# Optimization experiments

Hardware: AMD Instinct MI355X
Metric: run time of the kernel (lower is better)

Reference implementation:

```python
import jax, jax.numpy as jnp
import numpy as np

B, T, IN = 32, 1024, 256
H = 128          # hidden_size
NL = 2           # num_layers
NC = 4           # num_classes
F2 = 2 * H       # bidirectional feature size


def _lstm_dir(xs, w_ih, w_hh, b_ih, b_hh, reverse):
    # xs: [T, B, in]; w_ih: [4H, in]; w_hh: [4H, H]
    if reverse:
        xs = xs[::-1]
    h0 = jnp.zeros((xs.shape[1], H), xs.dtype)
    c0 = jnp.zeros((xs.shape[1], H), xs.dtype)

    def step(carry, xt):
        h, c = carry
        g = xt @ w_ih.T + b_ih + h @ w_hh.T + b_hh  # [B, 4H]
        i, f, gg, o = jnp.split(g, 4, axis=-1)       # PyTorch gate order i,f,g,o
        c = jax.nn.sigmoid(f) * c + jax.nn.sigmoid(i) * jnp.tanh(gg)
        h = jax.nn.sigmoid(o) * jnp.tanh(c)
        return (h, c), h

    _, hs = jax.lax.scan(step, (h0, c0), xs)  # [T, B, H]
    if reverse:
        hs = hs[::-1]
    return hs


def setup_inputs() -> dict:
    key = jax.random.key(0)
    ks = jax.random.split(key, 12)
    s = 0.05
    x = jax.random.normal(ks[0], (B, T, IN), jnp.float32)
    # stacked LSTM params: [layer, direction, ...]; layer0 in = IN, layer1 in = 2H = IN
    w_ih = jax.random.normal(ks[1], (NL, 2, 4 * H, IN), jnp.float32) * s
    w_hh = jax.random.normal(ks[2], (NL, 2, 4 * H, H), jnp.float32) * s
    b_ih = jax.random.normal(ks[3], (NL, 2, 4 * H), jnp.float32) * s
    b_hh = jax.random.normal(ks[4], (NL, 2, 4 * H), jnp.float32) * s
    wq = jax.random.normal(ks[5], (F2, F2), jnp.float32) * s
    wk = jax.random.normal(ks[6], (F2, F2), jnp.float32) * s
    wv = jax.random.normal(ks[7], (F2, F2), jnp.float32) * s
    bq = jax.random.normal(ks[8], (F2,), jnp.float32) * s
    bk = jax.random.normal(ks[9], (F2,), jnp.float32) * s
    bv = jax.random.normal(ks[10], (F2,), jnp.float32) * s
    w_fc = jax.random.normal(ks[11], (NC, F2), jnp.float32) * s
    b_fc = jnp.zeros((NC,), jnp.float32)
    return {"x": x, "w_ih": w_ih, "w_hh": w_hh, "b_ih": b_ih, "b_hh": b_hh,
            "wq": wq, "wk": wk, "wv": wv, "bq": bq, "bk": bk, "bv": bv,
            "w_fc": w_fc, "b_fc": b_fc}


def reference(x, w_ih, w_hh, b_ih, b_hh, wq, wk, wv, bq, bk, bv, w_fc, b_fc):
    # --- biLSTM (eval mode: inter-layer dropout inactive) ---
    xs = jnp.swapaxes(x, 0, 1)  # time-major [T, B, IN]
    for l in range(NL):
        fwd = _lstm_dir(xs, w_ih[l, 0], w_hh[l, 0], b_ih[l, 0], b_hh[l, 0], False)
        bwd = _lstm_dir(xs, w_ih[l, 1], w_hh[l, 1], b_ih[l, 1], b_hh[l, 1], True)
        xs = jnp.concatenate([fwd, bwd], axis=-1)  # [T, B, 2H]
    out = jnp.swapaxes(xs, 0, 1)  # [B, T, 2H]
    # --- naive full self-attention ---
    q = out @ wq.T + bq
    k = out @ wk.T + bk
    v = out @ wv.T + bv
    scores = jnp.einsum('btd,bsd->bts', q, k) / jnp.sqrt(jnp.float32(F2))
    attn = jax.nn.softmax(scores, axis=-1)          # [B, T, T]
    ctx = jnp.einsum('bts,bsd->btd', attn, v)       # [B, T, 2H]
    # --- FC head on last timestep ---
    return ctx[:, -1, :] @ w_fc.T + b_fc            # [B, NC]
```

## Files before the change

### kernel.cpp

```cpp
#include <hip/hip_runtime.h>
#include <math.h>
#include <stdint.h>

#define BB 32
#define TT 1024
#define HH 128
#define G4 512
#define CH 16
#define XPS 516

typedef _Float16 half2_t __attribute__((ext_vector_type(2)));
typedef _Float16 half8_t __attribute__((ext_vector_type(8)));
typedef float f32x4 __attribute__((ext_vector_type(4)));

__device__ __forceinline__ float fdot2f(half2_t a, half2_t b, float c) {
    return __builtin_amdgcn_fdot2(a, b, c, false);
}
__device__ __forceinline__ float rcpf(float x) {
    return __builtin_amdgcn_rcpf(x);
}
__device__ __forceinline__ float dpp_xor1(float x) {
    return __builtin_bit_cast(float, __builtin_amdgcn_update_dpp(
        0, __builtin_bit_cast(int, x), 0xB1, 0xF, 0xF, true));
}
__device__ __forceinline__ float dpp_xor2(float x) {
    return __builtin_bit_cast(float, __builtin_amdgcn_update_dpp(
        0, __builtin_bit_cast(int, x), 0x4E, 0xF, 0xF, true));
}
__device__ __forceinline__ void bar_lgkm() {
    asm volatile("s_waitcnt lgkmcnt(0)\n\ts_barrier" ::: "memory");
}

__global__ __launch_bounds__(256) void cvt_wih(
    const float* __restrict__ w, _Float16* __restrict__ o)
{
    const int i = (blockIdx.x * 256 + threadIdx.x) * 4;
    float4 f = *(const float4*)(w + i);
    half2_t t[2] = { half2_t{(_Float16)f.x, (_Float16)f.y},
                     half2_t{(_Float16)f.z, (_Float16)f.w} };
    *(float2*)(o + i) = *(float2*)t;
}

__global__ __launch_bounds__(512, 1) void lstm_fused(
    const float* __restrict__ x_in,
    const _Float16* __restrict__ wih16_l,
    const float* __restrict__ b_ih_l,
    const float* __restrict__ b_hh_l,
    const float* __restrict__ w_hh_l,
    float* __restrict__ out)
{
    const int b = blockIdx.x & 31;
    const int d = blockIdx.x >> 5;
    const int tid = threadIdx.x;
    const int wvid = tid >> 6;
    const int l = tid & 63;
    const int s = l & 3;
    const int g = l >> 2;
    const int j = (wvid << 4) | g;

    __shared__ __align__(16) _Float16 hs[HH];
    __shared__ __align__(16) float xp[2][CH * XPS];
    __shared__ __align__(16) half2_t xr[2][CH * 128];
    __shared__ __align__(16) float obuf[CH * HH];

    half2_t wv[4][16];
#pragma unroll
    for (int G = 0; G < 4; ++G) {
        const float* wr = w_hh_l + (size_t)(d * G4 + 128 * G + j) * HH + 32 * s;
#pragma unroll
        for (int q4 = 0; q4 < 8; ++q4) {
            float4 f = *(const float4*)(wr + 4 * q4);
            wv[G][2 * q4]     = half2_t{(_Float16)f.x, (_Float16)f.y};
            wv[G][2 * q4 + 1] = half2_t{(_Float16)f.z, (_Float16)f.w};
        }
    }

    const int acol0 = wvid * 64 + (l & 15);
    const _Float16* wn = wih16_l + ((size_t)d * G4 + acol0) * 256 + (l >> 4) * 8;
    const float bias0 = b_ih_l[d * G4 + acol0]      + b_hh_l[d * G4 + acol0];
    const float bias1 = b_ih_l[d * G4 + acol0 + 16] + b_hh_l[d * G4 + acol0 + 16];
    const float bias2 = b_ih_l[d * G4 + acol0 + 32] + b_hh_l[d * G4 + acol0 + 32];
    const float bias3 = b_ih_l[d * G4 + acol0 + 48] + b_hh_l[d * G4 + acol0 + 48];

    const int cbase = ((acol0 & 127) << 2) + (acol0 >> 7);

    const float* xbase = x_in + (size_t)b * TT * 256;

    const int a_noswz = (l & 15) * 512 + (l >> 4) * 16;
    const int a_swz   = (l & 7) << 4;
    const int w_swz_byte = (tid * 16) ^ (((tid >> 5) & 7) << 4);

#pragma unroll 1
    for (int p = 0; p < 2; ++p) {
        const int tlo = d ? (1008 - p * CH) : p * CH;
        const float* gs = xbase + (size_t)tlo * 256 + tid * 8;
        float4 f0 = *(const float4*)gs;
        float4 f1 = *(const float4*)(gs + 4);
        half2_t t4[4] = { half2_t{(_Float16)f0.x, (_Float16)f0.y},
                          half2_t{(_Float16)f0.z, (_Float16)f0.w},
                          half2_t{(_Float16)f1.x, (_Float16)f1.y},
                          half2_t{(_Float16)f1.z, (_Float16)f1.w} };
        *(float4*)((char*)xr[p] + w_swz_byte) = *(float4*)t4;
    }
    __syncthreads();

    f32x4 acc0 = {bias0, bias0, bias0, bias0};
    f32x4 acc1 = {bias1, bias1, bias1, bias1};
    f32x4 acc2 = {bias2, bias2, bias2, bias2};
    f32x4 acc3 = {bias3, bias3, bias3, bias3};

#pragma unroll
    for (int kt = 0; kt < 8; ++kt) {
        half8_t af = *(const half8_t*)((const char*)xr[0] + ((a_noswz + kt * 64) ^ a_swz));
        acc0 = __builtin_amdgcn_mfma_f32_16x16x32_f16(af, *(const half8_t*)(wn +         kt * 32), acc0, 0, 0, 0);
        acc1 = __builtin_amdgcn_mfma_f32_16x16x32_f16(af, *(const half8_t*)(wn +  4096 + kt * 32), acc1, 0, 0, 0);
        acc2 = __builtin_amdgcn_mfma_f32_16x16x32_f16(af, *(const half8_t*)(wn +  8192 + kt * 32), acc2, 0, 0, 0);
        acc3 = __builtin_amdgcn_mfma_f32_16x16x32_f16(af, *(const half8_t*)(wn + 12288 + kt * 32), acc3, 0, 0, 0);
    }
    {
        const int rb = (l >> 4) * 4;
#pragma unroll
        for (int q = 0; q < 4; ++q) {
            const int ix = (rb + q) * XPS + cbase;
            xp[0][ix]       = acc0[q];
            xp[0][ix + 64]  = acc1[q];
            xp[0][ix + 128] = acc2[q];
            xp[0][ix + 192] = acc3[q];
        }
    }
    acc0 = (f32x4){bias0, bias0, bias0, bias0};
    acc1 = (f32x4){bias1, bias1, bias1, bias1};
    acc2 = (f32x4){bias2, bias2, bias2, bias2};
    acc3 = (f32x4){bias3, bias3, bias3, bias3};

    if (tid < 64) ((half2_t*)hs)[tid] = half2_t{(_Float16)0.f, (_Float16)0.f};
    float c = 0.f;
    float* ob = out + (size_t)b * TT * 256 + d * HH;
    __syncthreads();

    float4 rg0 = {}, rg1 = {};
    half8_t afrag = {};
    for (int ck = 0; ck < 64; ++ck) {
        const int cur = ck & 1;
        const bool doproj = (ck + 1 < 64);
        if (ck + 2 < 64) {
            const int tlo2 = d ? (1008 - (ck + 2) * CH) : (ck + 2) * CH;
            const float* gs = xbase + (size_t)tlo2 * 256 + tid * 8;
            rg0 = *(const float4*)gs;
            rg1 = *(const float4*)(gs + 4);
        }
        const float* xb = xp[cur];
        const char* xr_rd = (const char*)xr[cur ^ 1];

#pragma unroll 1
        for (int si = 0; si < CH; ++si) {
            half8_t bA = {}, bB = {};
            if (doproj) {
                const int kt = si >> 1;
                if (!(si & 1)) {
                    afrag = *(const half8_t*)(xr_rd + ((a_noswz + kt * 64) ^ a_swz));
                    bA = *(const half8_t*)(wn +        kt * 32);
                    bB = *(const half8_t*)(wn + 4096 + kt * 32);
                } else {
                    bA = *(const half8_t*)(wn +  8192 + kt * 32);
                    bB = *(const half8_t*)(wn + 12288 + kt * 32);
                }
            }

            const int lds_t = d ? (CH - 1 - si) : si;

            const float4 xg4 = *(const float4*)&xb[lds_t * XPS + (j << 2)];

            const float4* hp = (const float4*)(hs + 32 * s);
            float4 hA = hp[0], hB = hp[1], hC = hp[2], hD = hp[3];
            half2_t hh[16];
            hh[0]  = __builtin_bit_cast(half2_t, hA.x);
            hh[1]  = __builtin_bit_cast(half2_t, hA.y);
            hh[2]  = __builtin_bit_cast(half2_t, hA.z);
            hh[3]  = __builtin_bit_cast(half2_t, hA.w);
            hh[4]  = __builtin_bit_cast(half2_t, hB.x);
            hh[5]  = __builtin_bit_cast(half2_t, hB.y);
            hh[6]  = __builtin_bit_cast(half2_t, hB.z);
            hh[7]  = __builtin_bit_cast(half2_t, hB.w);
            hh[8]  = __builtin_bit_cast(half2_t, hC.x);
            hh[9]  = __builtin_bit_cast(half2_t, hC.y);
            hh[10] = __builtin_bit_cast(half2_t, hC.z);
            hh[11] = __builtin_bit_cast(half2_t, hC.w);
            hh[12] = __builtin_bit_cast(half2_t, hD.x);
            hh[13] = __builtin_bit_cast(half2_t, hD.y);
            hh[14] = __builtin_bit_cast(half2_t, hD.z);
            hh[15] = __builtin_bit_cast(half2_t, hD.w);

            float a0 = 0.f, a1 = 0.f, a2 = 0.f, a3 = 0.f;
            float e0 = 0.f, e1 = 0.f, e2 = 0.f, e3 = 0.f;
#pragma unroll
            for (int kk = 0; kk < 8; ++kk) {
                a0 = fdot2f(wv[0][kk], hh[kk], a0);
                a1 = fdot2f(wv[1][kk], hh[kk], a1);
                a2 = fdot2f(wv[2][kk], hh[kk], a2);
                a3 = fdot2f(wv[3][kk], hh[kk], a3);
                e0 = fdot2f(wv[0][kk + 8], hh[kk + 8], e0);
                e1 = fdot2f(wv[1][kk + 8], hh[kk + 8], e1);
                e2 = fdot2f(wv[2][kk + 8], hh[kk + 8], e2);
                e3 = fdot2f(wv[3][kk + 8], hh[kk + 8], e3);
            }
            a0 += e0; a1 += e1; a2 += e2; a3 += e3;

            a0 += dpp_xor1(a0); a0 += dpp_xor2(a0);
            a1 += dpp_xor1(a1); a1 += dpp_xor2(a1);
            a2 += dpp_xor1(a2); a2 += dpp_xor2(a2);
            a3 += dpp_xor1(a3); a3 += dpp_xor2(a3);

            const float gi = rcpf(1.f + __expf(-(a0 + xg4.x)));
            const float gf = rcpf(1.f + __expf(-(a1 + xg4.y)));
            const float gg = 1.f - 2.f * rcpf(1.f + __expf(2.f * (a2 + xg4.z)));
            const float go = rcpf(1.f + __expf(-(a3 + xg4.w)));
            c = gf * c + gi * gg;
            const float th = 1.f - 2.f * rcpf(1.f + __expf(2.f * c));
            const float h = go * th;
            if (s == 0) {
                hs[j] = (_Float16)h;
                obuf[si * HH + j] = h;
            }

            if (doproj) {
                if (!(si & 1)) {
                    acc0 = __builtin_amdgcn_mfma_f32_16x16x32_f16(afrag, bA, acc0, 0, 0, 0);
                    acc1 = __builtin_amdgcn_mfma_f32_16x16x32_f16(afrag, bB, acc1, 0, 0, 0);
                } else {
                    acc2 = __builtin_amdgcn_mfma_f32_16x16x32_f16(afrag, bA, acc2, 0, 0, 0);
                    acc3 = __builtin_amdgcn_mfma_f32_16x16x32_f16(afrag, bB, acc3, 0, 0, 0);
                }
            }

            bar_lgkm();
        }

        {
            const int idx = tid * 4;
            const int sf = idx >> 7, jf = idx & 127;
            const int sg = ck * CH + sf;
            const int t  = d ? (TT - 1 - sg) : sg;
            float4 o0 = *(const float4*)&obuf[idx];
            *(float4*)&ob[(size_t)t * 256 + jf] = o0;
        }
        if (doproj) {
            float* xpn = xp[cur ^ 1];
            const int rb = (l >> 4) * 4;
#pragma unroll
            for (int q = 0; q < 4; ++q) {
                const int ix = (rb + q) * XPS + cbase;
                xpn[ix]       = acc0[q];
                xpn[ix + 64]  = acc1[q];
                xpn[ix + 128] = acc2[q];
                xpn[ix + 192] = acc3[q];
            }
            acc0 = (f32x4){bias0, bias0, bias0, bias0};
            acc1 = (f32x4){bias1, bias1, bias1, bias1};
            acc2 = (f32x4){bias2, bias2, bias2, bias2};
            acc3 = (f32x4){bias3, bias3, bias3, bias3};
        }
        if (ck + 2 < 64) {
            half2_t t4[4] = { half2_t{(_Float16)rg0.x, (_Float16)rg0.y},
                              half2_t{(_Float16)rg0.z, (_Float16)rg0.w},
                              half2_t{(_Float16)rg1.x, (_Float16)rg1.y},
                              half2_t{(_Float16)rg1.z, (_Float16)rg1.w} };
            *(float4*)((char*)xr[cur] + w_swz_byte) = *(float4*)t4;
        }
        __syncthreads();
    }
}

__global__ __launch_bounds__(1024) void attn_kernel(
    const float* __restrict__ out1,
    const float* __restrict__ wq, const float* __restrict__ bq,
    const float* __restrict__ wk,
    const float* __restrict__ wv, const float* __restrict__ bv,
    const float* __restrict__ wfc, const float* __restrict__ bfc,
    float* __restrict__ outp)
{
    const int b = blockIdx.x;
    const int tid = threadIdx.x;
    const int n = tid & 255, qq = tid >> 8;

    __shared__ float xl[256], q[256], u[256], cx[256];
    __shared__ __align__(16) float r[256];
    __shared__ float sc[TT];
    __shared__ float red[1024];
    __shared__ float part[4][256];

    const float* ob = out1 + (size_t)b * TT * 256;

    if (tid < 256) xl[tid] = ob[(size_t)(TT - 1) * 256 + tid];
    __syncthreads();

    {
        float a = 0.f;
        const float* wr = wq + (size_t)n * 256 + qq * 64;
        const float* xq = xl + qq * 64;
#pragma unroll 8
        for (int k = 0; k < 64; ++k) a += xq[k] * wr[k];
        part[qq][n] = a;
    }
    __syncthreads();
    if (tid < 256) q[tid] = bq[tid] + part[0][tid] + part[1][tid] + part[2][tid] + part[3][tid];
    __syncthreads();

    {
        float a = 0.f;
        const float* wkp = wk + (size_t)(qq * 64) * 256 + n;
#pragma unroll 8
        for (int dd = 0; dd < 64; ++dd) a += q[qq * 64 + dd] * wkp[(size_t)dd * 256];
        part[qq][n] = a;
    }
    __syncthreads();
    if (tid < 256) r[tid] = part[0][tid] + part[1][tid] + part[2][tid] + part[3][tid];
    __syncthreads();

    {
        const int wave = tid >> 6, lane = tid & 63;
        float4 r4 = *(const float4*)&r[lane * 4];
        for (int t = wave; t < TT; t += 16) {
            float4 o4 = *(const float4*)(ob + (size_t)t * 256 + lane * 4);
            float p = r4.x * o4.x + r4.y * o4.y + r4.z * o4.z + r4.w * o4.w;
#pragma unroll
            for (int off = 32; off > 0; off >>= 1) p += __shfl_down(p, off, 64);
            if (lane == 0) sc[t] = p * 0.0625f;
        }
    }
    __syncthreads();

    float v = sc[tid];
    red[tid] = v; __syncthreads();
    for (int st = 512; st > 0; st >>= 1) {
        if (tid < st) red[tid] = fmaxf(red[tid], red[tid + st]);
        __syncthreads();
    }
    const float mx = red[0]; __syncthreads();
    const float e = expf(v - mx);
    sc[tid] = e;
    red[tid] = e; __syncthreads();
    for (int st = 512; st > 0; st >>= 1) {
        if (tid < st) red[tid] += red[tid + st];
        __syncthreads();
    }
    const float inv = 1.f / red[0];
    __syncthreads();

    {
        float a = 0.f;
        const float* op = ob + (size_t)(qq * 256) * 256 + n;
        const float* sp = sc + qq * 256;
#pragma unroll 4
        for (int t = 0; t < 256; ++t) a += sp[t] * op[(size_t)t * 256];
        part[qq][n] = a;
    }
    __syncthreads();
    if (tid < 256) u[tid] = (part[0][tid] + part[1][tid] + part[2][tid] + part[3][tid]) * inv;
    __syncthreads();

    {
        float a = 0.f;
        const float* wr = wv + (size_t)n * 256 + qq * 64;
#pragma unroll 8
        for (int k = 0; k < 64; ++k) a += u[qq * 64 + k] * wr[k];
        part[qq][n] = a;
    }
    __syncthreads();
    if (tid < 256) cx[tid] = bv[tid] + part[0][tid] + part[1][tid] + part[2][tid] + part[3][tid];
    __syncthreads();

    if (tid < 4) {
        float o = bfc[tid];
        for (int k = 0; k < 256; ++k) o += cx[k] * wfc[tid * 256 + k];
        outp[b * 4 + tid] = o;
    }
}

extern "C" void kernel_launch(void* const* d_in, const int* in_sizes, int n_in,
                              void* d_out, int out_size, void* d_ws, size_t ws_size,
                              hipStream_t stream)
{
    const float* x    = (const float*)d_in[0];
    const float* w_ih = (const float*)d_in[1];
    const float* w_hh = (const float*)d_in[2];
    const float* b_ih = (const float*)d_in[3];
    const float* b_hh = (const float*)d_in[4];
    const float* wq   = (const float*)d_in[5];
    const float* wk   = (const float*)d_in[6];
    const float* wv   = (const float*)d_in[7];
    const float* bq   = (const float*)d_in[8];
    const float* bv   = (const float*)d_in[10];
    const float* wfc  = (const float*)d_in[11];
    const float* bfcv = (const float*)d_in[12];
    float* outp = (float*)d_out;

    float* ws = (float*)d_ws;
    _Float16* wih16 = (_Float16*)ws;
    float* out0 = ws + 262144;
    float* out1 = out0 + 8388608;

    cvt_wih<<<512, 256, 0, stream>>>(w_ih, wih16);

    lstm_fused<<<64, 512, 0, stream>>>(x, wih16, b_ih, b_hh, w_hh, out0);
    lstm_fused<<<64, 512, 0, stream>>>(out0, wih16 + 262144, b_ih + 1024, b_hh + 1024,
                                       w_hh + 2 * 512 * 128, out1);
    attn_kernel<<<32, 1024, 0, stream>>>(out1, wq, bq, wk, wv, bv, wfc, bfcv, outp);
}
```

Baseline: 1.745 ms.

## Split LSTM block into dedicated recurrent and projection wavefronts

Adds two producer wavefronts per block that compute the input-gate projection with MFMA for the next chunk, while eight wavefronts run only the serial recurrence. Barrier counts are matched so both groups step in lockstep. The goal is to take the MFMA loads and issue off the latency-critical recurrent step. In exchange the block grows to 640 threads, the projection waves carry 16 accumulators and so more register pressure, and the barrier matching between the two roles is fragile.

Result: slower. 3.369 ms (+93.0%).

```diff
diff --git a/kernel.cpp b/kernel.cpp
--- a/kernel.cpp
+++ b/kernel.cpp
@@ -29,6 +29,9 @@
 }
 __device__ __forceinline__ void bar_lgkm() {
     asm volatile("s_waitcnt lgkmcnt(0)\n\ts_barrier" ::: "memory");
+}
+__device__ __forceinline__ void bar_full() {
+    asm volatile("s_waitcnt vmcnt(0) lgkmcnt(0)\n\ts_barrier" ::: "memory");
 }
 
 __global__ __launch_bounds__(256) void cvt_wih(
@@ -41,7 +44,7 @@
     *(float2*)(o + i) = *(float2*)t;
 }
 
-__global__ __launch_bounds__(512, 1) void lstm_fused(
+__global__ __launch_bounds__(640) void lstm_fused(
     const float* __restrict__ x_in,
     const _Float16* __restrict__ wih16_l,
     const float* __restrict__ b_ih_l,
@@ -54,220 +57,219 @@
     const int tid = threadIdx.x;
     const int wvid = tid >> 6;
     const int l = tid & 63;
-    const int s = l & 3;
-    const int g = l >> 2;
-    const int j = (wvid << 4) | g;
+    const bool isrec = wvid < 8;
 
     __shared__ __align__(16) _Float16 hs[HH];
     __shared__ __align__(16) float xp[2][CH * XPS];
     __shared__ __align__(16) half2_t xr[2][CH * 128];
     __shared__ __align__(16) float obuf[CH * HH];
 
-    half2_t wv[4][16];
-#pragma unroll
-    for (int G = 0; G < 4; ++G) {
-        const float* wr = w_hh_l + (size_t)(d * G4 + 128 * G + j) * HH + 32 * s;
-#pragma unroll
-        for (int q4 = 0; q4 < 8; ++q4) {
-            float4 f = *(const float4*)(wr + 4 * q4);
-            wv[G][2 * q4]     = half2_t{(_Float16)f.x, (_Float16)f.y};
-            wv[G][2 * q4 + 1] = half2_t{(_Float16)f.z, (_Float16)f.w};
-        }
-    }
-
-    const int acol0 = wvid * 64 + (l & 15);
-    const _Float16* wn = wih16_l + ((size_t)d * G4 + acol0) * 256 + (l >> 4) * 8;
-    const float bias0 = b_ih_l[d * G4 + acol0]      + b_hh_l[d * G4 + acol0];
-    const float bias1 = b_ih_l[d * G4 + acol0 + 16] + b_hh_l[d * G4 + acol0 + 16];
-    const float bias2 = b_ih_l[d * G4 + acol0 + 32] + b_hh_l[d * G4 + acol0 + 32];
-    const float bias3 = b_ih_l[d * G4 + acol0 + 48] + b_hh_l[d * G4 + acol0 + 48];
-
-    const int cbase = ((acol0 & 127) << 2) + (acol0 >> 7);
-
     const float* xbase = x_in + (size_t)b * TT * 256;
 
     const int a_noswz = (l & 15) * 512 + (l >> 4) * 16;
     const int a_swz   = (l & 7) << 4;
     const int w_swz_byte = (tid * 16) ^ (((tid >> 5) & 7) << 4);
 
+    if (isrec) {
 #pragma unroll 1
-    for (int p = 0; p < 2; ++p) {
-        const int tlo = d ? (1008 - p * CH) : p * CH;
-        const float* gs = xbase + (size_t)tlo * 256 + tid * 8;
-        float4 f0 = *(const float4*)gs;
-        float4 f1 = *(const float4*)(gs + 4);
-        half2_t t4[4] = { half2_t{(_Float16)f0.x, (_Float16)f0.y},
-                          half2_t{(_Float16)f0.z, (_Float16)f0.w},
-                          half2_t{(_Float16)f1.x, (_Float16)f1.y},
-                          half2_t{(_Float16)f1.z, (_Float16)f1.w} };
-        *(float4*)((char*)xr[p] + w_swz_byte) = *(float4*)t4;
-    }
-    __syncthreads();
-
-    f32x4 acc0 = {bias0, bias0, bias0, bias0};
-    f32x4 acc1 = {bias1, bias1, bias1, bias1};
-    f32x4 acc2 = {bias2, bias2, bias2, bias2};
-    f32x4 acc3 = {bias3, bias3, bias3, bias3};
-
-#pragma unroll
-    for (int kt = 0; kt < 8; ++kt) {
-        half8_t af = *(const half8_t*)((const char*)xr[0] + ((a_noswz + kt * 64) ^ a_swz));
-        acc0 = __builtin_amdgcn_mfma_f32_16x16x32_f16(af, *(const half8_t*)(wn +         kt * 32), acc0, 0, 0, 0);
-        acc1 = __builtin_amdgcn_mfma_f32_16x16x32_f16(af, *(const half8_t*)(wn +  4096 + kt * 32), acc1, 0, 0, 0);
-        acc2 = __builtin_amdgcn_mfma_f32_16x16x32_f16(af, *(const half8_t*)(wn +  8192 + kt * 32), acc2, 0, 0, 0);
-        acc3 = __builtin_amdgcn_mfma_f32_16x16x32_f16(af, *(const half8_t*)(wn + 12288 + kt * 32), acc3, 0, 0, 0);
-    }
-    {
+        for (int p = 0; p < 2; ++p) {
+            const int tlo = d ? (1008 - p * CH) : p * CH;
+            const float* gs = xbase + (size_t)tlo * 256 + tid * 8;
+            float4 f0 = *(const float4*)gs;
+            float4 f1 = *(const float4*)(gs + 4);
+            half2_t t4[4] = { half2_t{(_Float16)f0.x, (_Float16)f0.y},
+                              half2_t{(_Float16)f0.z, (_Float16)f0.w},
+                              half2_t{(_Float16)f1.x, (_Float16)f1.y},
+                              half2_t{(_Float16)f1.z, (_Float16)f1.w} };
+            *(float4*)((char*)xr[p] + w_swz_byte) = *(float4*)t4;
+        }
+        if (tid < 64) ((half2_t*)hs)[tid] = half2_t{(_Float16)0.f, (_Float16)0.f};
+    }
+    __syncthreads();
+
+    if (isrec) {
+        const int s = l & 3;
+        const int g = l >> 2;
+        const int j = (wvid << 4) | g;
+
+        half2_t wv[4][16];
+#pragma unroll
+        for (int G = 0; G < 4; ++G) {
+            const float* wr = w_hh_l + (size_t)(d * G4 + 128 * G + j) * HH + 32 * s;
+#pragma unroll
+            for (int q4 = 0; q4 < 8; ++q4) {
+                float4 f = *(const float4*)(wr + 4 * q4);
+                wv[G][2 * q4]     = half2_t{(_Float16)f.x, (_Float16)f.y};
+                wv[G][2 * q4 + 1] = half2_t{(_Float16)f.z, (_Float16)f.w};
+            }
+        }
+        float c = 0.f;
+        float* ob = out + (size_t)b * TT * 256 + d * HH;
+
+        __syncthreads();
+
+        float4 rg0 = {}, rg1 = {};
+#pragma unroll 1
+        for (int ck = 0; ck < 64; ++ck) {
+            const int cur = ck & 1;
+            if (ck + 2 < 64) {
+                const int tlo2 = d ? (1008 - (ck + 2) * CH) : (ck + 2) * CH;
+                const float* gs = xbase + (size_t)tlo2 * 256 + tid * 8;
+                rg0 = *(const float4*)gs;
+                rg1 = *(const float4*)(gs + 4);
+            }
+            const float* xb = xp[cur];
+
+#pragma unroll 1
+            for (int si = 0; si < CH; ++si) {
+                const int lds_t = d ? (CH - 1 - si) : si;
+                const float4 xg4 = *(const float4*)&xb[lds_t * XPS + (j << 2)];
+
+                const float4* hp = (const float4*)(hs + 32 * s);
+                float4 hA = hp[0], hB = hp[1], hC = hp[2], hD = hp[3];
+                half2_t hh[16];
+                hh[0]  = __builtin_bit_cast(half2_t, hA.x);
+                hh[1]  = __builtin_bit_cast(half2_t, hA.y);
+                hh[2]  = __builtin_bit_cast(half2_t, hA.z);
+                hh[3]  = __builtin_bit_cast(half2_t, hA.w);
+                hh[4]  = __builtin_bit_cast(half2_t, hB.x);
+                hh[5]  = __builtin_bit_cast(half2_t, hB.y);
+                hh[6]  = __builtin_bit_cast(half2_t, hB.z);
+                hh[7]  = __builtin_bit_cast(half2_t, hB.w);
+                hh[8]  = __builtin_bit_cast(half2_t, hC.x);
+                hh[9]  = __builtin_bit_cast(half2_t, hC.y);
+                hh[10] = __builtin_bit_cast(half2_t, hC.z);
+                hh[11] = __builtin_bit_cast(half2_t, hC.w);
+                hh[12] = __builtin_bit_cast(half2_t, hD.x);
+                hh[13] = __builtin_bit_cast(half2_t, hD.y);
+                hh[14] = __builtin_bit_cast(half2_t, hD.z);
+                hh[15] = __builtin_bit_cast(half2_t, hD.w);
+
+                float a0 = 0.f, a1 = 0.f, a2 = 0.f, a3 = 0.f;
+                float e0 = 0.f, e1 = 0.f, e2 = 0.f, e3 = 0.f;
+#pragma unroll
+                for (int kk = 0; kk < 8; ++kk) {
+                    a0 = fdot2f(wv[0][kk], hh[kk], a0);
+                    a1 = fdot2f(wv[1][kk], hh[kk], a1);
+                    a2 = fdot2f(wv[2][kk], hh[kk], a2);
+                    a3 = fdot2f(wv[3][kk], hh[kk], a3);
+                    e0 = fdot2f(wv[0][kk + 8], hh[kk + 8], e0);
+                    e1 = fdot2f(wv[1][kk + 8], hh[kk + 8], e1);
+                    e2 = fdot2f(wv[2][kk + 8], hh[kk + 8], e2);
+                    e3 = fdot2f(wv[3][kk + 8], hh[kk + 8], e3);
+                }
+                a0 += e0; a1 += e1; a2 += e2; a3 += e3;
+
+                a0 += dpp_xor1(a0); a0 += dpp_xor2(a0);
+                a1 += dpp_xor1(a1); a1 += dpp_xor2(a1);
+                a2 += dpp_xor1(a2); a2 += dpp_xor2(a2);
+                a3 += dpp_xor1(a3); a3 += dpp_xor2(a3);
+
+                const float gi = rcpf(1.f + __expf(-(a0 + xg4.x)));
+                const float gf = rcpf(1.f + __expf(-(a1 + xg4.y)));
+                const float gg = 1.f - 2.f * rcpf(1.f + __expf(2.f * (a2 + xg4.z)));
+                const float go = rcpf(1.f + __expf(-(a3 + xg4.w)));
+                c = gf * c + gi * gg;
+                const float th = 1.f - 2.f * rcpf(1.f + __expf(2.f * c));
+                const float h = go * th;
+                if (s == 0) {
+                    hs[j] = (_Float16)h;
+                    obuf[si * HH + j] = h;
+                }
+                bar_lgkm();
+            }
+
+            {
+                const int idx = tid * 4;
+                const int sf = idx >> 7, jf = idx & 127;
+                const int sg = ck * CH + sf;
+                const int t  = d ? (TT - 1 - sg) : sg;
+                float4 o0 = *(const float4*)&obuf[idx];
+                *(float4*)&ob[(size_t)t * 256 + jf] = o0;
+            }
+            if (ck + 2 < 64) {
+                half2_t t4[4] = { half2_t{(_Float16)rg0.x, (_Float16)rg0.y},
+                                  half2_t{(_Float16)rg0.z, (_Float16)rg0.w},
+                                  half2_t{(_Float16)rg1.x, (_Float16)rg1.y},
+                                  half2_t{(_Float16)rg1.z, (_Float16)rg1.w} };
+                *(float4*)((char*)xr[cur] + w_swz_byte) = *(float4*)t4;
+            }
+            bar_full();
+        }
+    } else {
+        const int pwave = wvid - 8;
+        const int pcol0 = pwave * 256 + (l & 15);
+        const _Float16* wn = wih16_l + ((size_t)d * G4 + pcol0) * 256 + (l >> 4) * 8;
+        float bias[16];
+        int cix[16];
+#pragma unroll
+        for (int nt = 0; nt < 16; ++nt) {
+            const int n = pcol0 + 16 * nt;
+            bias[nt] = b_ih_l[d * G4 + n] + b_hh_l[d * G4 + n];
+            cix[nt] = ((n & 127) << 2) + (n >> 7);
+        }
         const int rb = (l >> 4) * 4;
-#pragma unroll
-        for (int q = 0; q < 4; ++q) {
-            const int ix = (rb + q) * XPS + cbase;
-            xp[0][ix]       = acc0[q];
-            xp[0][ix + 64]  = acc1[q];
-            xp[0][ix + 128] = acc2[q];
-            xp[0][ix + 192] = acc3[q];
-        }
-    }
-    acc0 = (f32x4){bias0, bias0, bias0, bias0};
-    acc1 = (f32x4){bias1, bias1, bias1, bias1};
-    acc2 = (f32x4){bias2, bias2, bias2, bias2};
-    acc3 = (f32x4){bias3, bias3, bias3, bias3};
-
-    if (tid < 64) ((half2_t*)hs)[tid] = half2_t{(_Float16)0.f, (_Float16)0.f};
-    float c = 0.f;
-    float* ob = out + (size_t)b * TT * 256 + d * HH;
-    __syncthreads();
-
-    float4 rg0 = {}, rg1 = {};
-    half8_t afrag = {};
-    for (int ck = 0; ck < 64; ++ck) {
-        const int cur = ck & 1;
-        const bool doproj = (ck + 1 < 64);
-        if (ck + 2 < 64) {
-            const int tlo2 = d ? (1008 - (ck + 2) * CH) : (ck + 2) * CH;
-            const float* gs = xbase + (size_t)tlo2 * 256 + tid * 8;
-            rg0 = *(const float4*)gs;
-            rg1 = *(const float4*)(gs + 4);
-        }
-        const float* xb = xp[cur];
-        const char* xr_rd = (const char*)xr[cur ^ 1];
+
+        f32x4 acc[16];
+#pragma unroll
+        for (int nt = 0; nt < 16; ++nt) acc[nt] = (f32x4){bias[nt], bias[nt], bias[nt], bias[nt]};
+
+#pragma unroll
+        for (int kt = 0; kt < 8; ++kt) {
+            half8_t af = *(const half8_t*)((const char*)xr[0] + ((a_noswz + kt * 64) ^ a_swz));
+#pragma unroll
+            for (int nt = 0; nt < 16; ++nt)
+                acc[nt] = __builtin_amdgcn_mfma_f32_16x16x32_f16(
+                    af, *(const half8_t*)(wn + nt * 4096 + kt * 32), acc[nt], 0, 0, 0);
+        }
+#pragma unroll
+        for (int nt = 0; nt < 16; ++nt) {
+#pragma unroll
+            for (int qq = 0; qq < 4; ++qq)
+                xp[0][(rb + qq) * XPS + cix[nt]] = acc[nt][qq];
+            acc[nt] = (f32x4){bias[nt], bias[nt], bias[nt], bias[nt]};
+        }
+
+        __syncthreads();
 
 #pragma unroll 1
-        for (int si = 0; si < CH; ++si) {
-            half8_t bA = {}, bB = {};
+        for (int ck = 0; ck < 64; ++ck) {
+            const int cur = ck & 1;
+            const bool doproj = (ck + 1 < 64);
+            const char* xr_rd = (const char*)xr[cur ^ 1];
+
             if (doproj) {
-                const int kt = si >> 1;
-                if (!(si & 1)) {
-                    afrag = *(const half8_t*)(xr_rd + ((a_noswz + kt * 64) ^ a_swz));
-                    bA = *(const half8_t*)(wn +        kt * 32);
-                    bB = *(const half8_t*)(wn + 4096 + kt * 32);
-                } else {
-                    bA = *(const half8_t*)(wn +  8192 + kt * 32);
-                    bB = *(const half8_t*)(wn + 12288 + kt * 32);
+                half8_t afrag = {};
+#pragma unroll
+                for (int slot = 0; slot < CH; ++slot) {
+                    const int kt = slot >> 1;
+                    const int hbase = (slot & 1) * 8;
+                    if (!(slot & 1))
+                        afrag = *(const half8_t*)(xr_rd + ((a_noswz + kt * 64) ^ a_swz));
+                    half8_t bf[8];
+#pragma unroll
+                    for (int i = 0; i < 8; ++i)
+                        bf[i] = *(const half8_t*)(wn + (hbase + i) * 4096 + kt * 32);
+#pragma unroll
+                    for (int i = 0; i < 8; ++i)
+                        acc[hbase + i] = __builtin_amdgcn_mfma_f32_16x16x32_f16(
+                            afrag, bf[i], acc[hbase + i], 0, 0, 0);
+                    bar_lgkm();
                 }
-            }
-
-            const int lds_t = d ? (CH - 1 - si) : si;
-
-            const float4 xg4 = *(const float4*)&xb[lds_t * XPS + (j << 2)];
-
-            const float4* hp = (const float4*)(hs + 32 * s);
-            float4 hA = hp[0], hB = hp[1], hC = hp[2], hD = hp[3];
-            half2_t hh[16];
-            hh[0]  = __builtin_bit_cast(half2_t, hA.x);
-            hh[1]  = __builtin_bit_cast(half2_t, hA.y);
-            hh[2]  = __builtin_bit_cast(half2_t, hA.z);
-            hh[3]  = __builtin_bit_cast(half2_t, hA.w);
-            hh[4]  = __builtin_bit_cast(half2_t, hB.x);
-            hh[5]  = __builtin_bit_cast(half2_t, hB.y);
-            hh[6]  = __builtin_bit_cast(half2_t, hB.z);
-            hh[7]  = __builtin_bit_cast(half2_t, hB.w);
-            hh[8]  = __builtin_bit_cast(half2_t, hC.x);
-            hh[9]  = __builtin_bit_cast(half2_t, hC.y);
-            hh[10] = __builtin_bit_cast(half2_t, hC.z);
-            hh[11] = __builtin_bit_cast(half2_t, hC.w);
-            hh[12] = __builtin_bit_cast(half2_t, hD.x);
-            hh[13] = __builtin_bit_cast(half2_t, hD.y);
-            hh[14] = __builtin_bit_cast(half2_t, hD.z);
-            hh[15] = __builtin_bit_cast(half2_t, hD.w);
-
-            float a0 = 0.f, a1 = 0.f, a2 = 0.f, a3 = 0.f;
-            float e0 = 0.f, e1 = 0.f, e2 = 0.f, e3 = 0.f;
-#pragma unroll
-            for (int kk = 0; kk < 8; ++kk) {
-                a0 = fdot2f(wv[0][kk], hh[kk], a0);
-                a1 = fdot2f(wv[1][kk], hh[kk], a1);
-                a2 = fdot2f(wv[2][kk], hh[kk], a2);
-                a3 = fdot2f(wv[3][kk], hh[kk], a3);
-                e0 = fdot2f(wv[0][kk + 8], hh[kk + 8], e0);
-                e1 = fdot2f(wv[1][kk + 8], hh[kk + 8], e1);
-                e2 = fdot2f(wv[2][kk + 8], hh[kk + 8], e2);
-                e3 = fdot2f(wv[3][kk + 8], hh[kk + 8], e3);
-            }
-            a0 += e0; a1 += e1; a2 += e2; a3 += e3;
-
-            a0 += dpp_xor1(a0); a0 += dpp_xor2(a0);
-            a1 += dpp_xor1(a1); a1 += dpp_xor2(a1);
-            a2 += dpp_xor1(a2); a2 += dpp_xor2(a2);
-            a3 += dpp_xor1(a3); a3 += dpp_xor2(a3);
-
-            const float gi = rcpf(1.f + __expf(-(a0 + xg4.x)));
-            const float gf = rcpf(1.f + __expf(-(a1 + xg4.y)));
-            const float gg = 1.f - 2.f * rcpf(1.f + __expf(2.f * (a2 + xg4.z)));
-            const float go = rcpf(1.f + __expf(-(a3 + xg4.w)));
-            c = gf * c + gi * gg;
-            const float th = 1.f - 2.f * rcpf(1.f + __expf(2.f * c));
-            const float h = go * th;
-            if (s == 0) {
-                hs[j] = (_Float16)h;
-                obuf[si * HH + j] = h;
-            }
-
-            if (doproj) {
-                if (!(si & 1)) {
-                    acc0 = __builtin_amdgcn_mfma_f32_16x16x32_f16(afrag, bA, acc0, 0, 0, 0);
-                    acc1 = __builtin_amdgcn_mfma_f32_16x16x32_f16(afrag, bB, acc1, 0, 0, 0);
-                } else {
-                    acc2 = __builtin_amdgcn_mfma_f32_16x16x32_f16(afrag, bA, acc2, 0, 0, 0);
-                    acc3 = __builtin_amdgcn_mfma_f32_16x16x32_f16(afrag, bB, acc3, 0, 0, 0);
+                float* xpn = xp[cur ^ 1];
+#pragma unroll
+                for (int nt = 0; nt < 16; ++nt) {
+#pragma unroll
+                    for (int qq = 0; qq < 4; ++qq)
+                        xpn[(rb + qq) * XPS + cix[nt]] = acc[nt][qq];
+                    acc[nt] = (f32x4){bias[nt], bias[nt], bias[nt], bias[nt]};
                 }
-            }
-
-            bar_lgkm();
-        }
-
-        {
-            const int idx = tid * 4;
-            const int sf = idx >> 7, jf = idx & 127;
-            const int sg = ck * CH + sf;
-            const int t  = d ? (TT - 1 - sg) : sg;
-            float4 o0 = *(const float4*)&obuf[idx];
-            *(float4*)&ob[(size_t)t * 256 + jf] = o0;
-        }
-        if (doproj) {
-            float* xpn = xp[cur ^ 1];
-            const int rb = (l >> 4) * 4;
-#pragma unroll
-            for (int q = 0; q < 4; ++q) {
-                const int ix = (rb + q) * XPS + cbase;
-                xpn[ix]       = acc0[q];
-                xpn[ix + 64]  = acc1[q];
-                xpn[ix + 128] = acc2[q];
-                xpn[ix + 192] = acc3[q];
-            }
-            acc0 = (f32x4){bias0, bias0, bias0, bias0};
-            acc1 = (f32x4){bias1, bias1, bias1, bias1};
-            acc2 = (f32x4){bias2, bias2, bias2, bias2};
-            acc3 = (f32x4){bias3, bias3, bias3, bias3};
-        }
-        if (ck + 2 < 64) {
-            half2_t t4[4] = { half2_t{(_Float16)rg0.x, (_Float16)rg0.y},
-                              half2_t{(_Float16)rg0.z, (_Float16)rg0.w},
-                              half2_t{(_Float16)rg1.x, (_Float16)rg1.y},
-                              half2_t{(_Float16)rg1.z, (_Float16)rg1.w} };
-            *(float4*)((char*)xr[cur] + w_swz_byte) = *(float4*)t4;
-        }
-        __syncthreads();
+            } else {
+#pragma unroll
+                for (int slot = 0; slot < CH; ++slot) bar_lgkm();
+            }
+            bar_full();
+        }
     }
 }
 
@@ -402,8 +404,8 @@
 
     cvt_wih<<<512, 256, 0, stream>>>(w_ih, wih16);
 
-    lstm_fused<<<64, 512, 0, stream>>>(x, wih16, b_ih, b_hh, w_hh, out0);
-    lstm_fused<<<64, 512, 0, stream>>>(out0, wih16 + 262144, b_ih + 1024, b_hh + 1024,
+    lstm_fused<<<64, 640, 0, stream>>>(x, wih16, b_ih, b_hh, w_hh, out0);
+    lstm_fused<<<64, 640, 0, stream>>>(out0, wih16 + 262144, b_ih + 1024, b_hh + 1024,
                                        w_hh + 2 * 512 * 128, out1);
     attn_kernel<<<32, 1024, 0, stream>>>(out1, wq, bq, wk, wv, bv, wfc, bfcv, outp);
 }
```
